# Kernel tuning notes

Measured on AMD Instinct MI355X. Metric: run time of the kernel, lower is better.

## Reference

```python
import jax, jax.numpy as jnp
import numpy as np

DT = 0.01          # oscillator integration step
GPI_TAU = 0.01     # gpi accumulation rate
NOISE_TAU = 1.0    # noise scale
MIN_OMEGA, MAX_OMEGA = 0.1, 1.0


def clinear(xr, xi, Wr, Wi, br, bi):
    # complex linear: (Wr + i Wi)(xr + i xi) + (br + i bi), weights stored [out, in]
    yr = xr @ Wr.T - xi @ Wi.T + br
    yi = xr @ Wi.T + xi @ Wr.T + bi
    return yr, yi


def crelu(yr, yi):
    # ReLU applied to real and imaginary parts independently
    return jax.nn.relu(yr), jax.nn.relu(yi)


def hopf_step(xr, xi, r, phi, omega):
    # Hopf oscillator in polar form, forced by complex input x = xr + i xi:
    #   dr   = dt * ( r(1 - r^2) + Re(x e^{-i phi}) )
    #   dphi = dt * ( omega + Im(x e^{-i phi}) / r )
    # output = r_new * e^{i phi_new}
    c, s = jnp.cos(phi), jnp.sin(phi)
    r_new = r + DT * (r * (1.0 - r * r) + xr * c + xi * s)
    phi_new = phi + DT * (omega + (xi * c - xr * s) / jnp.maximum(r, 1e-6))
    return r_new * jnp.cos(phi_new), r_new * jnp.sin(phi_new), r_new, phi_new


def setup_inputs() -> dict:
    T, D, U, A = 4096, 256, 2048, 64
    key = jax.random.key(0)
    ks = jax.random.split(key, 16)

    def lin(k, out_d, in_d):
        k1, k2, k3, k4 = jax.random.split(k, 4)
        sc = 1.0 / np.sqrt(in_d)
        return (jax.random.normal(k1, (out_d, in_d), dtype=jnp.float32) * sc,
                jax.random.normal(k2, (out_d, in_d), dtype=jnp.float32) * sc,
                jax.random.normal(k3, (out_d,), dtype=jnp.float32) * sc,
                jax.random.normal(k4, (out_d,), dtype=jnp.float32) * sc)

    l1Wr, l1Wi, l1br, l1bi = lin(ks[0], U, D)
    dpWr, dpWi, dpbr, dpbi = lin(ks[1], A, U)
    ipWr, ipWi, ipbr, ipbi = lin(ks[2], A, U)
    cWr, cWi, cbr, cbi = lin(ks[3], 1, U)
    return {
        'state': jax.random.normal(ks[4], (T, 1, D), dtype=jnp.float32),
        'phi1_init': jax.random.uniform(ks[5], (1, U), dtype=jnp.float32),
        'phi2_init': jax.random.uniform(ks[6], (1, U), dtype=jnp.float32),
        'noise_u': jax.random.uniform(ks[7], (T, A), dtype=jnp.float32),
        'omega1': jax.random.uniform(ks[8], (U,), minval=MIN_OMEGA, maxval=MAX_OMEGA, dtype=jnp.float32),
        'omega2': jax.random.uniform(ks[9], (U,), minval=MIN_OMEGA, maxval=MAX_OMEGA, dtype=jnp.float32),
        'l1Wr': l1Wr, 'l1Wi': l1Wi, 'l1br': l1br, 'l1bi': l1bi,
        'dpWr': dpWr, 'dpWi': dpWi, 'dpbr': dpbr, 'dpbi': dpbi,
        'ipWr': ipWr, 'ipWi': ipWi, 'ipbr': ipbr, 'ipbi': ipbi,
        'cWr': cWr, 'cWi': cWi, 'cbr': cbr, 'cbi': cbi,
    }


def reference(state, phi1_init, phi2_init, noise_u, omega1, omega2,
              l1Wr, l1Wi, l1br, l1bi, dpWr, dpWi, dpbr, dpbi,
              ipWr, ipWi, ipbr, ipbi, cWr, cWi, cbr, cbi):
    U = l1Wr.shape[0]
    A = dpWr.shape[0]
    carry0 = (jnp.ones((1, U)), phi1_init * 0.1,   # r1, phi1 (torch.rand/10)
              jnp.ones((1, U)), phi2_init * 0.1,   # r2, phi2
              jnp.zeros((1, A)),                   # gpi
              jnp.zeros((1, 1)))                   # p_value

    def step(carry, xs):
        r1, phi1, r2, phi2, gpi, p_value = carry
        s_t, nz_t = xs  # s_t: [1, D], nz_t: [A]
        # x = cReLU(l1(complex(state[t], state[t])))
        xr, xi = crelu(*clinear(s_t, s_t, l1Wr, l1Wi, l1br, l1bi))
        d1r, d1i, r1, phi1 = hopf_step(xr, xi, r1, phi1, omega1)
        d2r, d2i, r2, phi2 = hopf_step(xr, xi, r2, phi2, omega2)
        vr, vi = clinear(d1r, d1i, cWr, cWi, cbr, cbi)
        value = jnp.sqrt(vr * vr + vi * vi)          # |critic(d1out)|  [1,1]
        delta_V = value - p_value                    # pd_flag = sc_flag = 0
        lD1 = jax.nn.sigmoid(5.0 * delta_V)
        lD2 = jax.nn.sigmoid(-5.0 * delta_V)
        dpr, dpi = crelu(*clinear(d1r * lD1, d1i * lD1, dpWr, dpWi, dpbr, dpbi))
        ipr, ipi = crelu(*clinear(d2r * lD2, d2i * lD2, ipWr, ipWi, ipbr, ipbi))
        noise = NOISE_TAU * (nz_t[None, :] * 2.0 * lD2 - lD2)  # real-valued, adds to real part
        diff_r = dpr - (ipr + noise)
        diff_i = dpi - ipi
        gpi = gpi + GPI_TAU * jnp.sqrt(diff_r * diff_r + diff_i * diff_i)
        return (r1, phi1, r2, phi2, gpi, value), (gpi, value)

    (r1, phi1, r2, phi2, gpi, value), (gpi_traj, value_traj) = jax.lax.scan(
        step, carry0, (state, noise_u))
    probs = jax.nn.softmax(gpi, axis=1)
    return probs, value, gpi_traj
```

## Files before the change

kernel.cpp:

```cpp
#include <hip/hip_runtime.h>
#include <hip/hip_bf16.h>
#include <stdint.h>


#define T_ 4096
#define D_ 256
#define U_ 2048
#define A_ 64

typedef float f32x4 __attribute__((ext_vector_type(4)));

__device__ __forceinline__ uint32_t pack2(float lo, float hi) {
  __hip_bfloat16 l = __float2bfloat16(lo);
  __hip_bfloat16 h = __float2bfloat16(hi);
  uint16_t lu, hu;
  __builtin_memcpy(&lu, &l, 2);
  __builtin_memcpy(&hu, &h, 2);
  return (uint32_t)lu | ((uint32_t)hu << 16);
}
__device__ __forceinline__ float bflo(uint32_t p) { return __uint_as_float(p << 16); }
__device__ __forceinline__ float bfhi(uint32_t p) { return __uint_as_float(p & 0xffff0000u); }

#define HOPF_LOAD(BUF, i, tbase)                                            \
  do {                                                                      \
    const float* bx_ = xc + (size_t)((tbase) + (i)) * (U_ * 2);             \
    asm volatile("global_load_dwordx2 %0, %1, %2"                           \
                 : "=v"(BUF[i])                                             \
                 : "v"(voffx), "s"(bx_));                                   \
  } while (0)

#define HOPF_STEP(BUF, i, tb)                                               \
  do {                                                                      \
    const float xr_ = BUF[i].x, xi_ = BUF[i].y;                             \
    const float f_ = fmaf(xr_, c, xi_ * s);                                 \
    const float g_ = fmaf(xi_, c, -(xr_ * s));                              \
    const float rn_ = fmaf(0.01f, fmaf(r, fmaf(-r, r, 1.0f), f_), r);       \
    const float rinv_ = __builtin_amdgcn_rcpf(fmaxf(r, 1e-6f));             \
    const float phin_ = fmaf(0.01f, g_ * rinv_, phi + dto);                 \
    float cn_, sn_;                                                         \
    __sincosf(phin_, &sn_, &cn_);                                           \
    uint32_t pk_;                                                           \
    asm("v_cvt_pk_bf16_f32 %0, %1, %2"                                     \
        : "=v"(pk_)                                                         \
        : "v"(rn_ * cn_), "v"(rn_ * sn_));                                  \
    const uint32_t* bd_ = dst + (size_t)((tb) + (i)) * U_;                  \
    asm volatile("global_store_dword %0, %1, %2" ::"v"(voffd), "v"(pk_),    \
                 "s"(bd_));                                                  \
    r = rn_; phi = phin_; c = cn_; s = sn_;                                 \
  } while (0)

#define VMWAIT(N)                                  \
  asm volatile("s_waitcnt vmcnt(" #N ")");         \
  __builtin_amdgcn_sched_barrier(0)

#define WAIT_TILE(tt)                                                       \
  do {                                                                      \
    uint32_t rdy_;                                                          \
    for (;;) {                                                              \
      rdy_ = 0u;                                                            \
      if (threadIdx.x == 0)                                                 \
        rdy_ = __hip_atomic_fetch_add(&flags[tt], 0u, __ATOMIC_RELAXED,     \
                                      __HIP_MEMORY_SCOPE_AGENT);            \
      rdy_ = __shfl(rdy_, 0);                                               \
      if (rdy_ >= 32u) break;                                               \
      __builtin_amdgcn_s_sleep(8);                                          \
    }                                                                       \
    __builtin_amdgcn_sched_barrier(0);                                      \
  } while (0)

__global__ __launch_bounds__(256) void k_g1hopf(
    const float* __restrict__ S, const float* __restrict__ Wr,
    const float* __restrict__ Wi, const float* __restrict__ br,
    const float* __restrict__ bi, const float* __restrict__ phi1,
    const float* __restrict__ phi2, const float* __restrict__ om1,
    const float* __restrict__ om2, float* __restrict__ xc,
    uint32_t* __restrict__ d1c, uint32_t* __restrict__ d2c,
    uint32_t* __restrict__ flags) {
  const int bid = blockIdx.x;
  if (bid >= 64) {
    __shared__ float sT[32][68];
    __shared__ float wrT[32][68];
    __shared__ float wiT[32][68];
    const int tid = threadIdx.x;
    const int gb = bid - 64;
    const int t0 = (gb >> 5) * 64;
    const int u0 = (gb & 31) * 64;
    const int un = tid & 15, tm = tid >> 4;
    const int lr = tid >> 3;
    const int lc = (tid & 7) * 4;
    float accR[4][4] = {}, accI[4][4] = {};
    for (int k0 = 0; k0 < D_; k0 += 32) {
      __syncthreads();
#pragma unroll
      for (int p = 0; p < 2; ++p) {
        const int row = p * 32 + lr;
        float4 v = *(const float4*)&S[(size_t)(t0 + row) * D_ + k0 + lc];
        sT[lc + 0][row] = v.x; sT[lc + 1][row] = v.y;
        sT[lc + 2][row] = v.z; sT[lc + 3][row] = v.w;
        float4 a = *(const float4*)&Wr[(size_t)(u0 + row) * D_ + k0 + lc];
        wrT[lc + 0][row] = a.x; wrT[lc + 1][row] = a.y;
        wrT[lc + 2][row] = a.z; wrT[lc + 3][row] = a.w;
        float4 b = *(const float4*)&Wi[(size_t)(u0 + row) * D_ + k0 + lc];
        wiT[lc + 0][row] = b.x; wiT[lc + 1][row] = b.y;
        wiT[lc + 2][row] = b.z; wiT[lc + 3][row] = b.w;
      }
      __syncthreads();
#pragma unroll
      for (int k = 0; k < 32; ++k) {
        const float4 sv = *(const float4*)&sT[k][tm * 4];
        const float4 ar = *(const float4*)&wrT[k][un * 4];
        const float4 ai = *(const float4*)&wiT[k][un * 4];
        const float ss[4] = {sv.x, sv.y, sv.z, sv.w};
        const float wd[4] = {ar.x - ai.x, ar.y - ai.y, ar.z - ai.z, ar.w - ai.w};
        const float wm[4] = {ar.x + ai.x, ar.y + ai.y, ar.z + ai.z, ar.w + ai.w};
#pragma unroll
        for (int i = 0; i < 4; ++i)
#pragma unroll
          for (int j = 0; j < 4; ++j) {
            accR[i][j] = fmaf(ss[i], wd[j], accR[i][j]);
            accI[i][j] = fmaf(ss[i], wm[j], accI[i][j]);
          }
      }
    }
    const float4 brv = *(const float4*)&br[u0 + un * 4];
    const float4 biv = *(const float4*)&bi[u0 + un * 4];
    const float brx[4] = {brv.x, brv.y, brv.z, brv.w};
    const float bix[4] = {biv.x, biv.y, biv.z, biv.w};
#pragma unroll
    for (int i = 0; i < 4; ++i) {
      float vr[4], vi[4];
#pragma unroll
      for (int j = 0; j < 4; ++j) {
        vr[j] = fmaxf(accR[i][j] + brx[j], 0.f);
        vi[j] = fmaxf(accI[i][j] + bix[j], 0.f);
      }
      const size_t base = ((size_t)(t0 + tm * 4 + i) * U_ + u0 + un * 4) * 2;
      f32x4 lo = {vr[0], vi[0], vr[1], vi[1]};
      f32x4 hi = {vr[2], vi[2], vr[3], vi[3]};
      float* p0 = &xc[base];
      float* p1 = &xc[base + 4];
      asm volatile("global_store_dwordx4 %0, %1, off sc1" ::"v"(p0), "v"(lo)
                   : "memory");
      asm volatile("global_store_dwordx4 %0, %1, off sc1" ::"v"(p1), "v"(hi)
                   : "memory");
    }
    asm volatile("s_waitcnt vmcnt(0)");
    __syncthreads();
    if (tid == 0)
      __hip_atomic_fetch_add(&flags[t0 >> 6], 1u, __ATOMIC_RELAXED,
                             __HIP_MEMORY_SCOPE_AGENT);
    return;
  }
  if (threadIdx.x >= 64) return;
  __builtin_amdgcn_s_setprio(3);
  const int ub = bid & 31;
  const int osc = bid >> 5;
  const int u = ub * 64 + threadIdx.x;
  float phi = (osc ? phi2[u] : phi1[u]) * 0.1f;
  const float omega = osc ? om2[u] : om1[u];
  const uint32_t* __restrict__ dst = (osc ? d2c : d1c);
  const float dto = 0.01f * omega;
  float r = 1.0f;
  float c, s;
  __sincosf(phi, &s, &c);
  const uint32_t voffx = (uint32_t)u * 8u;
  const uint32_t voffd = (uint32_t)u * 4u;

  constexpr int PF = 32;
  float2 bufA[PF], bufB[PF];
  WAIT_TILE(0);
#pragma unroll
  for (int i = 0; i < PF; ++i) HOPF_LOAD(bufA, i, 0);
#pragma unroll
  for (int i = 0; i < PF; ++i) HOPF_LOAD(bufB, i, PF);
  VMWAIT(32);

  for (int t0 = 0; t0 < T_; t0 += 2 * PF) {
#pragma unroll
    for (int i = 0; i < PF; ++i) HOPF_STEP(bufA, i, t0);
    {
      int tp = t0 + 2 * PF;
      if (tp >= T_) tp = 0;
      WAIT_TILE(tp >> 6);
#pragma unroll
      for (int i = 0; i < PF; ++i) HOPF_LOAD(bufA, i, tp);
    }
    VMWAIT(63);
#pragma unroll
    for (int i = 0; i < PF; ++i) HOPF_STEP(bufB, i, t0 + PF);
    {
      int tp = t0 + 3 * PF;
      if (tp >= T_) tp = 0;
#pragma unroll
      for (int i = 0; i < PF; ++i) HOPF_LOAD(bufB, i, tp);
    }
    VMWAIT(63);
  }
  asm volatile("s_waitcnt vmcnt(0)");
  __builtin_amdgcn_s_setprio(0);
}

__global__ __launch_bounds__(256) void k_critic(
    const uint32_t* __restrict__ d1c, const float* __restrict__ cWr,
    const float* __restrict__ cWi, const float* __restrict__ cbr,
    const float* __restrict__ cbi, float* __restrict__ value) {
  const int t = blockIdx.x;
  const int tid = threadIdx.x;
  float vr = 0.f, vi = 0.f;
#pragma unroll
  for (int i = 0; i < 8; ++i) {
    const int uu = i * 256 + tid;
    const uint32_t p = d1c[(size_t)t * U_ + uu];
    const float dr = bflo(p), di = bfhi(p);
    const float wr = cWr[uu], wi = cWi[uu];
    vr = fmaf(dr, wr, fmaf(-di, wi, vr));
    vi = fmaf(dr, wi, fmaf(di, wr, vi));
  }
#pragma unroll
  for (int o = 32; o >= 1; o >>= 1) {
    vr += __shfl_xor(vr, o);
    vi += __shfl_xor(vi, o);
  }
  __shared__ float red[2][4];
  if ((tid & 63) == 0) { red[0][tid >> 6] = vr; red[1][tid >> 6] = vi; }
  __syncthreads();
  if (tid == 0) {
    const float r0 = red[0][0] + red[0][1] + red[0][2] + red[0][3] + cbr[0];
    const float i0 = red[1][0] + red[1][1] + red[1][2] + red[1][3] + cbi[0];
    value[t] = sqrtf(r0 * r0 + i0 * i0);
  }
}

__global__ __launch_bounds__(256) void k_ld(const float* __restrict__ value,
                                            float* __restrict__ lD1,
                                            float* __restrict__ lD2) {
  const int t = blockIdx.x * 256 + threadIdx.x;
  const float v = value[t];
  const float pv = (t > 0) ? value[t - 1] : 0.f;
  const float x = 5.0f * (v - pv);
  const float sg = 1.0f / (1.0f + __expf(-x));
  lD1[t] = sg;
  lD2[t] = 1.0f - sg;
}

__global__ __launch_bounds__(256) void k_gemmD(
    const uint32_t* __restrict__ d1c, const uint32_t* __restrict__ d2c,
    const float* __restrict__ dpWr, const float* __restrict__ dpWi,
    const float* __restrict__ ipWr, const float* __restrict__ ipWi,
    float* __restrict__ mpart) {
  __shared__ uint32_t d1T[32][68];
  __shared__ uint32_t d2T[32][68];
  __shared__ float w1r[32][68], w1i[32][68], w2r[32][68], w2i[32][68];
  const int tid = threadIdx.x;
  const int t0 = blockIdx.x * 64;
  const int ks = blockIdx.y;
  const int kb = ks * 512;
  const int an = tid & 15, tm = tid >> 4;
  const int lr = tid >> 3, lc = (tid & 7) * 4;
  float a1r[4][4] = {}, a1i[4][4] = {}, a2r[4][4] = {}, a2i[4][4] = {};
  for (int kc = 0; kc < 512; kc += 32) {
    __syncthreads();
#pragma unroll
    for (int p = 0; p < 2; ++p) {
      const int row = p * 32 + lr;
      const int col = kb + kc + lc;
      uint4 v1 = *(const uint4*)&d1c[(size_t)(t0 + row) * U_ + col];
      d1T[lc + 0][row] = v1.x; d1T[lc + 1][row] = v1.y;
      d1T[lc + 2][row] = v1.z; d1T[lc + 3][row] = v1.w;
      uint4 v2 = *(const uint4*)&d2c[(size_t)(t0 + row) * U_ + col];
      d2T[lc + 0][row] = v2.x; d2T[lc + 1][row] = v2.y;
      d2T[lc + 2][row] = v2.z; d2T[lc + 3][row] = v2.w;
      float4 f;
      f = *(const float4*)&dpWr[(size_t)row * U_ + col];
      w1r[lc + 0][row] = f.x; w1r[lc + 1][row] = f.y;
      w1r[lc + 2][row] = f.z; w1r[lc + 3][row] = f.w;
      f = *(const float4*)&dpWi[(size_t)row * U_ + col];
      w1i[lc + 0][row] = f.x; w1i[lc + 1][row] = f.y;
      w1i[lc + 2][row] = f.z; w1i[lc + 3][row] = f.w;
      f = *(const float4*)&ipWr[(size_t)row * U_ + col];
      w2r[lc + 0][row] = f.x; w2r[lc + 1][row] = f.y;
      w2r[lc + 2][row] = f.z; w2r[lc + 3][row] = f.w;
      f = *(const float4*)&ipWi[(size_t)row * U_ + col];
      w2i[lc + 0][row] = f.x; w2i[lc + 1][row] = f.y;
      w2i[lc + 2][row] = f.z; w2i[lc + 3][row] = f.w;
    }
    __syncthreads();
#pragma unroll
    for (int k = 0; k < 32; ++k) {
      const uint4 p1 = *(const uint4*)&d1T[k][tm * 4];
      const uint4 p2 = *(const uint4*)&d2T[k][tm * 4];
      const float4 q1r = *(const float4*)&w1r[k][an * 4];
      const float4 q1i = *(const float4*)&w1i[k][an * 4];
      const float4 q2r = *(const float4*)&w2r[k][an * 4];
      const float4 q2i = *(const float4*)&w2i[k][an * 4];
      const float d1r_[4] = {bflo(p1.x), bflo(p1.y), bflo(p1.z), bflo(p1.w)};
      const float d1i_[4] = {bfhi(p1.x), bfhi(p1.y), bfhi(p1.z), bfhi(p1.w)};
      const float d2r_[4] = {bflo(p2.x), bflo(p2.y), bflo(p2.z), bflo(p2.w)};
      const float d2i_[4] = {bfhi(p2.x), bfhi(p2.y), bfhi(p2.z), bfhi(p2.w)};
      const float u1r[4] = {q1r.x, q1r.y, q1r.z, q1r.w};
      const float u1i[4] = {q1i.x, q1i.y, q1i.z, q1i.w};
      const float u2r[4] = {q2r.x, q2r.y, q2r.z, q2r.w};
      const float u2i[4] = {q2i.x, q2i.y, q2i.z, q2i.w};
#pragma unroll
      for (int i = 0; i < 4; ++i)
#pragma unroll
        for (int j = 0; j < 4; ++j) {
          a1r[i][j] = fmaf(d1r_[i], u1r[j], fmaf(-d1i_[i], u1i[j], a1r[i][j]));
          a1i[i][j] = fmaf(d1r_[i], u1i[j], fmaf(d1i_[i], u1r[j], a1i[i][j]));
          a2r[i][j] = fmaf(d2r_[i], u2r[j], fmaf(-d2i_[i], u2i[j], a2r[i][j]));
          a2i[i][j] = fmaf(d2r_[i], u2i[j], fmaf(d2i_[i], u2r[j], a2i[i][j]));
        }
    }
  }
  const size_t MS = (size_t)T_ * A_;
#pragma unroll
  for (int i = 0; i < 4; ++i) {
    const size_t base = (size_t)(t0 + tm * 4 + i) * A_ + an * 4;
    *(float4*)&mpart[(size_t)(0 * 4 + ks) * MS + base] =
        make_float4(a1r[i][0], a1r[i][1], a1r[i][2], a1r[i][3]);
    *(float4*)&mpart[(size_t)(1 * 4 + ks) * MS + base] =
        make_float4(a1i[i][0], a1i[i][1], a1i[i][2], a1i[i][3]);
    *(float4*)&mpart[(size_t)(2 * 4 + ks) * MS + base] =
        make_float4(a2r[i][0], a2r[i][1], a2r[i][2], a2r[i][3]);
    *(float4*)&mpart[(size_t)(3 * 4 + ks) * MS + base] =
        make_float4(a2i[i][0], a2i[i][1], a2i[i][2], a2i[i][3]);
  }
}

__global__ __launch_bounds__(256) void k_epi(
    const float* __restrict__ mpart, const float* __restrict__ lD1,
    const float* __restrict__ lD2, const float* __restrict__ noise,
    const float* __restrict__ dpbr, const float* __restrict__ dpbi,
    const float* __restrict__ ipbr, const float* __restrict__ ipbi,
    float* __restrict__ nrm) {
  const size_t MS = (size_t)T_ * A_;
  const int gid = blockIdx.x * 256 + threadIdx.x;
  const size_t e0 = (size_t)gid * 4;
  const int t = (int)(e0 >> 6);
  const int a0 = (int)(e0 & 63);
  float m[4][4];
#pragma unroll
  for (int mi = 0; mi < 4; ++mi) {
    float4 acc = *(const float4*)&mpart[(size_t)(mi * 4 + 0) * MS + e0];
#pragma unroll
    for (int ksi = 1; ksi < 4; ++ksi) {
      const float4 v = *(const float4*)&mpart[(size_t)(mi * 4 + ksi) * MS + e0];
      acc.x += v.x; acc.y += v.y; acc.z += v.z; acc.w += v.w;
    }
    m[mi][0] = acc.x; m[mi][1] = acc.y; m[mi][2] = acc.z; m[mi][3] = acc.w;
  }
  const float l1 = lD1[t], l2 = lD2[t];
  const float4 nzv = *(const float4*)&noise[e0];
  const float nz[4] = {nzv.x, nzv.y, nzv.z, nzv.w};
  const float4 q1 = *(const float4*)&dpbr[a0];
  const float4 q2 = *(const float4*)&dpbi[a0];
  const float4 q3 = *(const float4*)&ipbr[a0];
  const float4 q4 = *(const float4*)&ipbi[a0];
  const float b1r[4] = {q1.x, q1.y, q1.z, q1.w};
  const float b1i[4] = {q2.x, q2.y, q2.z, q2.w};
  const float b2r[4] = {q3.x, q3.y, q3.z, q3.w};
  const float b2i[4] = {q4.x, q4.y, q4.z, q4.w};
  float res[4];
#pragma unroll
  for (int j = 0; j < 4; ++j) {
    const float dpr = fmaxf(fmaf(l1, m[0][j], b1r[j]), 0.f);
    const float dpi = fmaxf(fmaf(l1, m[1][j], b1i[j]), 0.f);
    const float ipr = fmaxf(fmaf(l2, m[2][j], b2r[j]), 0.f);
    const float ipi = fmaxf(fmaf(l2, m[3][j], b2i[j]), 0.f);
    const float nzs = l2 * (2.f * nz[j] - 1.f);
    const float dr = dpr - ipr - nzs;
    const float di = dpi - ipi;
    res[j] = sqrtf(dr * dr + di * di);
  }
  *(float4*)&nrm[e0] = make_float4(res[0], res[1], res[2], res[3]);
}

__global__ __launch_bounds__(64) void k_scan_part(const float* __restrict__ nrm,
                                                  float* __restrict__ csum) {
  const int c = blockIdx.x;
  const int a = threadIdx.x;
  const int tb = c * 64;
  float run = 0.f;
  for (int i = 0; i < 64; ++i) run += nrm[(size_t)(tb + i) * 64 + a];
  csum[c * 64 + a] = run;
}

__global__ __launch_bounds__(64) void k_scan_mid(const float* __restrict__ csum,
                                                 const float* __restrict__ value,
                                                 float* __restrict__ coff,
                                                 float* __restrict__ out) {
  const int a = threadIdx.x;
  float acc = 0.f;
#pragma unroll
  for (int cc = 0; cc < 64; ++cc) {
    coff[cc * 64 + a] = acc;
    acc += csum[cc * 64 + a];
  }
  const float g = 0.01f * acc;
  float mx = g;
#pragma unroll
  for (int o = 32; o >= 1; o >>= 1) mx = fmaxf(mx, __shfl_xor(mx, o));
  const float e = __expf(g - mx);
  float sm = e;
#pragma unroll
  for (int o = 32; o >= 1; o >>= 1) sm += __shfl_xor(sm, o);
  out[a] = e / sm;
  if (a == 0) out[64] = value[T_ - 1];
}

__global__ __launch_bounds__(64) void k_scan_out(const float* __restrict__ nrm,
                                                 const float* __restrict__ coff,
                                                 float* __restrict__ out) {
  const int c = blockIdx.x;
  const int a = threadIdx.x;
  const int tb = c * 64;
  float off = coff[c * 64 + a];
  float* o65 = out + 65;
  for (int i = 0; i < 64; ++i) {
    off += nrm[(size_t)(tb + i) * 64 + a];
    o65[(size_t)(tb + i) * 64 + a] = 0.01f * off;
  }
}

extern "C" void kernel_launch(void* const* d_in, const int* in_sizes, int n_in,
                              void* d_out, int out_size, void* d_ws,
                              size_t ws_size, hipStream_t stream) {
  const float* state = (const float*)d_in[0];
  const float* phi1 = (const float*)d_in[1];
  const float* phi2 = (const float*)d_in[2];
  const float* noise = (const float*)d_in[3];
  const float* om1 = (const float*)d_in[4];
  const float* om2 = (const float*)d_in[5];
  const float* l1Wr = (const float*)d_in[6];
  const float* l1Wi = (const float*)d_in[7];
  const float* l1br = (const float*)d_in[8];
  const float* l1bi = (const float*)d_in[9];
  const float* dpWr = (const float*)d_in[10];
  const float* dpWi = (const float*)d_in[11];
  const float* dpbr = (const float*)d_in[12];
  const float* dpbi = (const float*)d_in[13];
  const float* ipWr = (const float*)d_in[14];
  const float* ipWi = (const float*)d_in[15];
  const float* ipbr = (const float*)d_in[16];
  const float* ipbi = (const float*)d_in[17];
  const float* cWr = (const float*)d_in[18];
  const float* cWi = (const float*)d_in[19];
  const float* cbr = (const float*)d_in[20];
  const float* cbi = (const float*)d_in[21];
  float* out = (float*)d_out;

  char* ws = (char*)d_ws;
  float* xc = (float*)(ws + (size_t)0);
  uint32_t* d1c = (uint32_t*)(ws + (size_t)67108864);
  uint32_t* d2c = (uint32_t*)(ws + (size_t)100663296);
  float* mpart = (float*)(ws + (size_t)0);
  float* nrm = (float*)(ws + (size_t)16777216);
  float* value = (float*)(ws + (size_t)17825792);
  float* lD1 = (float*)(ws + (size_t)17825792 + 16384);
  float* lD2 = (float*)(ws + (size_t)17825792 + 32768);
  float* csum = (float*)(ws + (size_t)17825792 + 49152);
  float* coff = (float*)(ws + (size_t)17825792 + 65536);
  uint32_t* flags = (uint32_t*)out;

  hipMemsetAsync(out, 0, 256, stream);
  k_g1hopf<<<64 + (T_ / 64) * (U_ / 64), 256, 0, stream>>>(
      state, l1Wr, l1Wi, l1br, l1bi, phi1, phi2, om1, om2, xc, d1c, d2c,
      flags);
  k_critic<<<T_, 256, 0, stream>>>(d1c, cWr, cWi, cbr, cbi, value);
  k_ld<<<T_ / 256, 256, 0, stream>>>(value, lD1, lD2);
  k_gemmD<<<dim3(T_ / 64, 4), 256, 0, stream>>>(d1c, d2c, dpWr, dpWi, ipWr,
                                                ipWi, mpart);
  k_epi<<<256, 256, 0, stream>>>(mpart, lD1, lD2, noise, dpbr, dpbi, ipbr,
                                 ipbi, nrm);
  k_scan_part<<<64, 64, 0, stream>>>(nrm, csum);
  k_scan_mid<<<1, 64, 0, stream>>>(csum, value, coff, out);
  k_scan_out<<<64, 64, 0, stream>>>(nrm, coff, out);
}
```

Measured before the change: 512.1 us.

## Move second-layer complex GEMM to bf16 MFMA with split-precision weights

Replaces the scalar FP32 LDS-tiled complex GEMM (with 4-way K split and partial-sum buffer) by a bf16 MFMA 16x16x32 kernel that covers the full K per block. The weights are converted into hi/lo bf16 pairs inside the critic kernel launch to keep near-fp32 accuracy. The lD sigmoid kernel is folded into extra blocks of the GEMM launch, and the epilogue no longer reduces K-split partials. This removes the scalar FMA cost and the partial-sum traffic, at the price of redundant weight reads per block and no LDS reuse.

```diff
diff --git a/kernel.cpp b/kernel.cpp
--- a/kernel.cpp
+++ b/kernel.cpp
@@ -1,5 +1,6 @@
 #include <hip/hip_runtime.h>
 #include <hip/hip_bf16.h>
+#include <string.h>
 #include <stdint.h>
 
 
@@ -9,17 +10,17 @@
 #define A_ 64
 
 typedef float f32x4 __attribute__((ext_vector_type(4)));
-
-__device__ __forceinline__ uint32_t pack2(float lo, float hi) {
-  __hip_bfloat16 l = __float2bfloat16(lo);
-  __hip_bfloat16 h = __float2bfloat16(hi);
-  uint16_t lu, hu;
-  __builtin_memcpy(&lu, &l, 2);
-  __builtin_memcpy(&hu, &h, 2);
-  return (uint32_t)lu | ((uint32_t)hu << 16);
-}
+typedef short bh8 __attribute__((ext_vector_type(8)));
+union F8 { uint32_t u[4]; bh8 v; };
+
 __device__ __forceinline__ float bflo(uint32_t p) { return __uint_as_float(p << 16); }
 __device__ __forceinline__ float bfhi(uint32_t p) { return __uint_as_float(p & 0xffff0000u); }
+__device__ __forceinline__ uint16_t bf16rne(float x) {
+  __hip_bfloat16 h = __float2bfloat16(x);
+  uint16_t u;
+  __builtin_memcpy(&u, &h, 2);
+  return u;
+}
 
 #define HOPF_LOAD(BUF, i, tbase)                                            \
   do {                                                                      \
@@ -68,7 +69,7 @@
     __builtin_amdgcn_sched_barrier(0);                                      \
   } while (0)
 
-__global__ __launch_bounds__(256) void k_g1hopf(
+__global__ __launch_bounds__(256) void k_fused(
     const float* __restrict__ S, const float* __restrict__ Wr,
     const float* __restrict__ Wi, const float* __restrict__ br,
     const float* __restrict__ bi, const float* __restrict__ phi1,
@@ -200,12 +201,34 @@
   __builtin_amdgcn_s_setprio(0);
 }
 
-__global__ __launch_bounds__(256) void k_critic(
+__global__ __launch_bounds__(256) void k_crit_wcvt(
     const uint32_t* __restrict__ d1c, const float* __restrict__ cWr,
     const float* __restrict__ cWi, const float* __restrict__ cbr,
-    const float* __restrict__ cbi, float* __restrict__ value) {
+    const float* __restrict__ cbi, const float* __restrict__ dpWr,
+    const float* __restrict__ dpWi, const float* __restrict__ ipWr,
+    const float* __restrict__ ipWi, float* __restrict__ value,
+    uint16_t* __restrict__ wc) {
+  const int tid = threadIdx.x;
+  if (blockIdx.x >= T_) {
+    const float* srcs[4] = {dpWr, dpWi, ipWr, ipWi};
+    const int g = (blockIdx.x - T_) * 256 + tid;
+#pragma unroll
+    for (int mi = 0; mi < 4; ++mi) {
+      const float* sp = srcs[mi];
+      uint16_t* hi = wc + (size_t)(2 * mi) * 131072;
+      uint16_t* lo = wc + (size_t)(2 * mi + 1) * 131072;
+      for (int j = 0; j < 32; ++j) {
+        const int e = g * 32 + j;
+        const float w = sp[e];
+        const uint16_t hb = bf16rne(w);
+        const float hf = __uint_as_float((uint32_t)hb << 16);
+        hi[e] = hb;
+        lo[e] = bf16rne(w - hf);
+      }
+    }
+    return;
+  }
   const int t = blockIdx.x;
-  const int tid = threadIdx.x;
   float vr = 0.f, vi = 0.f;
 #pragma unroll
   for (int i = 0; i < 8; ++i) {
@@ -231,104 +254,99 @@
   }
 }
 
-__global__ __launch_bounds__(256) void k_ld(const float* __restrict__ value,
-                                            float* __restrict__ lD1,
-                                            float* __restrict__ lD2) {
-  const int t = blockIdx.x * 256 + threadIdx.x;
-  const float v = value[t];
-  const float pv = (t > 0) ? value[t - 1] : 0.f;
-  const float x = 5.0f * (v - pv);
-  const float sg = 1.0f / (1.0f + __expf(-x));
-  lD1[t] = sg;
-  lD2[t] = 1.0f - sg;
-}
-
-__global__ __launch_bounds__(256) void k_gemmD(
+#define MFMA_(A, B, C) \
+  __builtin_amdgcn_mfma_f32_16x16x32_bf16((A).v, (B).v, (C), 0, 0, 0)
+
+__global__ __launch_bounds__(256) void k_gemmDm_ld(
     const uint32_t* __restrict__ d1c, const uint32_t* __restrict__ d2c,
-    const float* __restrict__ dpWr, const float* __restrict__ dpWi,
-    const float* __restrict__ ipWr, const float* __restrict__ ipWi,
-    float* __restrict__ mpart) {
-  __shared__ uint32_t d1T[32][68];
-  __shared__ uint32_t d2T[32][68];
-  __shared__ float w1r[32][68], w1i[32][68], w2r[32][68], w2i[32][68];
+    const uint16_t* __restrict__ wc, const float* __restrict__ value,
+    float* __restrict__ m, float* __restrict__ lD1,
+    float* __restrict__ lD2) {
   const int tid = threadIdx.x;
-  const int t0 = blockIdx.x * 64;
-  const int ks = blockIdx.y;
-  const int kb = ks * 512;
-  const int an = tid & 15, tm = tid >> 4;
-  const int lr = tid >> 3, lc = (tid & 7) * 4;
-  float a1r[4][4] = {}, a1i[4][4] = {}, a2r[4][4] = {}, a2i[4][4] = {};
-  for (int kc = 0; kc < 512; kc += 32) {
-    __syncthreads();
-#pragma unroll
-    for (int p = 0; p < 2; ++p) {
-      const int row = p * 32 + lr;
-      const int col = kb + kc + lc;
-      uint4 v1 = *(const uint4*)&d1c[(size_t)(t0 + row) * U_ + col];
-      d1T[lc + 0][row] = v1.x; d1T[lc + 1][row] = v1.y;
-      d1T[lc + 2][row] = v1.z; d1T[lc + 3][row] = v1.w;
-      uint4 v2 = *(const uint4*)&d2c[(size_t)(t0 + row) * U_ + col];
-      d2T[lc + 0][row] = v2.x; d2T[lc + 1][row] = v2.y;
-      d2T[lc + 2][row] = v2.z; d2T[lc + 3][row] = v2.w;
-      float4 f;
-      f = *(const float4*)&dpWr[(size_t)row * U_ + col];
-      w1r[lc + 0][row] = f.x; w1r[lc + 1][row] = f.y;
-      w1r[lc + 2][row] = f.z; w1r[lc + 3][row] = f.w;
-      f = *(const float4*)&dpWi[(size_t)row * U_ + col];
-      w1i[lc + 0][row] = f.x; w1i[lc + 1][row] = f.y;
-      w1i[lc + 2][row] = f.z; w1i[lc + 3][row] = f.w;
-      f = *(const float4*)&ipWr[(size_t)row * U_ + col];
-      w2r[lc + 0][row] = f.x; w2r[lc + 1][row] = f.y;
-      w2r[lc + 2][row] = f.z; w2r[lc + 3][row] = f.w;
-      f = *(const float4*)&ipWi[(size_t)row * U_ + col];
-      w2i[lc + 0][row] = f.x; w2i[lc + 1][row] = f.y;
-      w2i[lc + 2][row] = f.z; w2i[lc + 3][row] = f.w;
-    }
-    __syncthreads();
-#pragma unroll
-    for (int k = 0; k < 32; ++k) {
-      const uint4 p1 = *(const uint4*)&d1T[k][tm * 4];
-      const uint4 p2 = *(const uint4*)&d2T[k][tm * 4];
-      const float4 q1r = *(const float4*)&w1r[k][an * 4];
-      const float4 q1i = *(const float4*)&w1i[k][an * 4];
-      const float4 q2r = *(const float4*)&w2r[k][an * 4];
-      const float4 q2i = *(const float4*)&w2i[k][an * 4];
-      const float d1r_[4] = {bflo(p1.x), bflo(p1.y), bflo(p1.z), bflo(p1.w)};
-      const float d1i_[4] = {bfhi(p1.x), bfhi(p1.y), bfhi(p1.z), bfhi(p1.w)};
-      const float d2r_[4] = {bflo(p2.x), bflo(p2.y), bflo(p2.z), bflo(p2.w)};
-      const float d2i_[4] = {bfhi(p2.x), bfhi(p2.y), bfhi(p2.z), bfhi(p2.w)};
-      const float u1r[4] = {q1r.x, q1r.y, q1r.z, q1r.w};
-      const float u1i[4] = {q1i.x, q1i.y, q1i.z, q1i.w};
-      const float u2r[4] = {q2r.x, q2r.y, q2r.z, q2r.w};
-      const float u2i[4] = {q2i.x, q2i.y, q2i.z, q2i.w};
-#pragma unroll
-      for (int i = 0; i < 4; ++i)
-#pragma unroll
-        for (int j = 0; j < 4; ++j) {
-          a1r[i][j] = fmaf(d1r_[i], u1r[j], fmaf(-d1i_[i], u1i[j], a1r[i][j]));
-          a1i[i][j] = fmaf(d1r_[i], u1i[j], fmaf(d1i_[i], u1r[j], a1i[i][j]));
-          a2r[i][j] = fmaf(d2r_[i], u2r[j], fmaf(-d2i_[i], u2i[j], a2r[i][j]));
-          a2i[i][j] = fmaf(d2r_[i], u2i[j], fmaf(d2i_[i], u2r[j], a2i[i][j]));
-        }
-    }
+  const int bid = blockIdx.x;
+  if (bid >= 256) {
+    const int t = (bid - 256) * 256 + tid;
+    const float v = value[t];
+    const float pv = (t > 0) ? value[t - 1] : 0.f;
+    const float x = 5.0f * (v - pv);
+    const float sg = 1.0f / (1.0f + __expf(-x));
+    lD1[t] = sg;
+    lD2[t] = 1.0f - sg;
+    return;
+  }
+  const int w = tid >> 6;
+  const int l = tid & 63;
+  const int t0 = bid * 16;
+  const int a0 = w * 16;
+  const int lr15 = l & 15;
+  const int g4 = (l >> 4) * 4;
+  const uint32_t* d1p = d1c + (size_t)(t0 + lr15) * U_ + g4;
+  const uint32_t* d2p = d2c + (size_t)(t0 + lr15) * U_ + g4;
+  const size_t wbase = (size_t)(a0 + lr15) * U_ + g4;
+  const uint16_t* w0 = wc + wbase;
+  f32x4 acc0 = {0.f, 0.f, 0.f, 0.f};
+  f32x4 acc1 = {0.f, 0.f, 0.f, 0.f};
+  f32x4 acc2 = {0.f, 0.f, 0.f, 0.f};
+  f32x4 acc3 = {0.f, 0.f, 0.f, 0.f};
+  for (int kk = 0; kk < U_; kk += 32) {
+    const uint4 da = *(const uint4*)(d1p + kk);
+    const uint4 db = *(const uint4*)(d1p + kk + 16);
+    F8 fr1, fi1, f1n;
+    fr1.u[0] = (da.x & 0xffffu) | (da.y << 16);
+    fr1.u[1] = (da.z & 0xffffu) | (da.w << 16);
+    fr1.u[2] = (db.x & 0xffffu) | (db.y << 16);
+    fr1.u[3] = (db.z & 0xffffu) | (db.w << 16);
+    fi1.u[0] = (da.x >> 16) | (da.y & 0xffff0000u);
+    fi1.u[1] = (da.z >> 16) | (da.w & 0xffff0000u);
+    fi1.u[2] = (db.x >> 16) | (db.y & 0xffff0000u);
+    fi1.u[3] = (db.z >> 16) | (db.w & 0xffff0000u);
+    f1n.u[0] = fi1.u[0] ^ 0x80008000u; f1n.u[1] = fi1.u[1] ^ 0x80008000u;
+    f1n.u[2] = fi1.u[2] ^ 0x80008000u; f1n.u[3] = fi1.u[3] ^ 0x80008000u;
+    const uint4 dc = *(const uint4*)(d2p + kk);
+    const uint4 dd = *(const uint4*)(d2p + kk + 16);
+    F8 fr2, fi2, f2n;
+    fr2.u[0] = (dc.x & 0xffffu) | (dc.y << 16);
+    fr2.u[1] = (dc.z & 0xffffu) | (dc.w << 16);
+    fr2.u[2] = (dd.x & 0xffffu) | (dd.y << 16);
+    fr2.u[3] = (dd.z & 0xffffu) | (dd.w << 16);
+    fi2.u[0] = (dc.x >> 16) | (dc.y & 0xffff0000u);
+    fi2.u[1] = (dc.z >> 16) | (dc.w & 0xffff0000u);
+    fi2.u[2] = (dd.x >> 16) | (dd.y & 0xffff0000u);
+    fi2.u[3] = (dd.z >> 16) | (dd.w & 0xffff0000u);
+    f2n.u[0] = fi2.u[0] ^ 0x80008000u; f2n.u[1] = fi2.u[1] ^ 0x80008000u;
+    f2n.u[2] = fi2.u[2] ^ 0x80008000u; f2n.u[3] = fi2.u[3] ^ 0x80008000u;
+    F8 wf[8];
+#pragma unroll
+    for (int ai = 0; ai < 8; ++ai) {
+      const uint16_t* bp = w0 + (size_t)ai * 131072 + kk;
+      const uint2 x0 = *(const uint2*)bp;
+      const uint2 x1 = *(const uint2*)(bp + 16);
+      wf[ai].u[0] = x0.x; wf[ai].u[1] = x0.y;
+      wf[ai].u[2] = x1.x; wf[ai].u[3] = x1.y;
+    }
+    acc0 = MFMA_(fr1, wf[0], acc0); acc0 = MFMA_(fr1, wf[1], acc0);
+    acc0 = MFMA_(f1n, wf[2], acc0); acc0 = MFMA_(f1n, wf[3], acc0);
+    acc1 = MFMA_(fr1, wf[2], acc1); acc1 = MFMA_(fr1, wf[3], acc1);
+    acc1 = MFMA_(fi1, wf[0], acc1); acc1 = MFMA_(fi1, wf[1], acc1);
+    acc2 = MFMA_(fr2, wf[4], acc2); acc2 = MFMA_(fr2, wf[5], acc2);
+    acc2 = MFMA_(f2n, wf[6], acc2); acc2 = MFMA_(f2n, wf[7], acc2);
+    acc3 = MFMA_(fr2, wf[6], acc3); acc3 = MFMA_(fr2, wf[7], acc3);
+    acc3 = MFMA_(fi2, wf[4], acc3); acc3 = MFMA_(fi2, wf[5], acc3);
   }
   const size_t MS = (size_t)T_ * A_;
 #pragma unroll
-  for (int i = 0; i < 4; ++i) {
-    const size_t base = (size_t)(t0 + tm * 4 + i) * A_ + an * 4;
-    *(float4*)&mpart[(size_t)(0 * 4 + ks) * MS + base] =
-        make_float4(a1r[i][0], a1r[i][1], a1r[i][2], a1r[i][3]);
-    *(float4*)&mpart[(size_t)(1 * 4 + ks) * MS + base] =
-        make_float4(a1i[i][0], a1i[i][1], a1i[i][2], a1i[i][3]);
-    *(float4*)&mpart[(size_t)(2 * 4 + ks) * MS + base] =
-        make_float4(a2r[i][0], a2r[i][1], a2r[i][2], a2r[i][3]);
-    *(float4*)&mpart[(size_t)(3 * 4 + ks) * MS + base] =
-        make_float4(a2i[i][0], a2i[i][1], a2i[i][2], a2i[i][3]);
+  for (int reg = 0; reg < 4; ++reg) {
+    const int t = t0 + (l >> 4) * 4 + reg;
+    const size_t o = (size_t)t * A_ + a0 + lr15;
+    m[0 * MS + o] = acc0[reg];
+    m[1 * MS + o] = acc1[reg];
+    m[2 * MS + o] = acc2[reg];
+    m[3 * MS + o] = acc3[reg];
   }
 }
 
 __global__ __launch_bounds__(256) void k_epi(
-    const float* __restrict__ mpart, const float* __restrict__ lD1,
+    const float* __restrict__ m4, const float* __restrict__ lD1,
     const float* __restrict__ lD2, const float* __restrict__ noise,
     const float* __restrict__ dpbr, const float* __restrict__ dpbi,
     const float* __restrict__ ipbr, const float* __restrict__ ipbi,
@@ -341,13 +359,8 @@
   float m[4][4];
 #pragma unroll
   for (int mi = 0; mi < 4; ++mi) {
-    float4 acc = *(const float4*)&mpart[(size_t)(mi * 4 + 0) * MS + e0];
-#pragma unroll
-    for (int ksi = 1; ksi < 4; ++ksi) {
-      const float4 v = *(const float4*)&mpart[(size_t)(mi * 4 + ksi) * MS + e0];
-      acc.x += v.x; acc.y += v.y; acc.z += v.z; acc.w += v.w;
-    }
-    m[mi][0] = acc.x; m[mi][1] = acc.y; m[mi][2] = acc.z; m[mi][3] = acc.w;
+    const float4 v = *(const float4*)&m4[(size_t)mi * MS + e0];
+    m[mi][0] = v.x; m[mi][1] = v.y; m[mi][2] = v.z; m[mi][3] = v.w;
   }
   const float l1 = lD1[t], l2 = lD2[t];
   const float4 nzv = *(const float4*)&noise[e0];
@@ -453,7 +466,8 @@
   float* xc = (float*)(ws + (size_t)0);
   uint32_t* d1c = (uint32_t*)(ws + (size_t)67108864);
   uint32_t* d2c = (uint32_t*)(ws + (size_t)100663296);
-  float* mpart = (float*)(ws + (size_t)0);
+  float* m4 = (float*)(ws + (size_t)0);
+  uint16_t* wc = (uint16_t*)(ws + (size_t)4194304);
   float* nrm = (float*)(ws + (size_t)16777216);
   float* value = (float*)(ws + (size_t)17825792);
   float* lD1 = (float*)(ws + (size_t)17825792 + 16384);
@@ -463,15 +477,15 @@
   uint32_t* flags = (uint32_t*)out;
 
   hipMemsetAsync(out, 0, 256, stream);
-  k_g1hopf<<<64 + (T_ / 64) * (U_ / 64), 256, 0, stream>>>(
+  k_fused<<<64 + (T_ / 64) * (U_ / 64), 256, 0, stream>>>(
       state, l1Wr, l1Wi, l1br, l1bi, phi1, phi2, om1, om2, xc, d1c, d2c,
       flags);
-  k_critic<<<T_, 256, 0, stream>>>(d1c, cWr, cWi, cbr, cbi, value);
-  k_ld<<<T_ / 256, 256, 0, stream>>>(value, lD1, lD2);
-  k_gemmD<<<dim3(T_ / 64, 4), 256, 0, stream>>>(d1c, d2c, dpWr, dpWi, ipWr,
-                                                ipWi, mpart);
-  k_epi<<<256, 256, 0, stream>>>(mpart, lD1, lD2, noise, dpbr, dpbi, ipbr,
-                                 ipbi, nrm);
+  k_crit_wcvt<<<T_ + 16, 256, 0, stream>>>(d1c, cWr, cWi, cbr, cbi, dpWr,
+                                           dpWi, ipWr, ipWi, value, wc);
+  k_gemmDm_ld<<<256 + 16, 256, 0, stream>>>(d1c, d2c, wc, value, m4, lD1,
+                                            lD2);
+  k_epi<<<256, 256, 0, stream>>>(m4, lD1, lD2, noise, dpbr, dpbi, ipbr, ipbi,
+                                 nrm);
   k_scan_part<<<64, 64, 0, stream>>>(nrm, csum);
   k_scan_mid<<<1, 64, 0, stream>>>(csum, value, coff, out);
   k_scan_out<<<64, 64, 0, stream>>>(nrm, coff, out);
```

After: 543.3 us. 6.1% more time.
